# Optimization experiments

Measured on AMD Instinct MI355X. Metric: run time of the kernel, lower is better.

## Reference

```python
import jax, jax.numpy as jnp
import numpy as np
import math

D_MODEL = 768
NHEAD = 12
D_HEAD = D_MODEL // NHEAD
TAU = 300.0
NEG = -1e9

def setup_inputs() -> dict:
    key = jax.random.key(0)
    ks = jax.random.split(key, 12)
    N, L, D = 64, 512, D_MODEL
    tokens = jax.random.normal(ks[0], (N, L, D), dtype=jnp.float32)
    ts = jax.random.uniform(ks[1], (N, L, 1), dtype=jnp.float32) * 3600.0  # seconds in a 1h window
    mask = jnp.ones((N, L, 1), dtype=jnp.float32)
    s = 1.0 / math.sqrt(D)
    Wq = jax.random.normal(ks[2], (D, D), dtype=jnp.float32) * s
    bq = jnp.zeros((D,), dtype=jnp.float32)
    Wk = jax.random.normal(ks[3], (D, D), dtype=jnp.float32) * s
    bk = jnp.zeros((D,), dtype=jnp.float32)
    Wv = jax.random.normal(ks[4], (D, D), dtype=jnp.float32) * s
    bv = jnp.zeros((D,), dtype=jnp.float32)
    Wo = jax.random.normal(ks[5], (D, D), dtype=jnp.float32) * s
    bo = jnp.zeros((D,), dtype=jnp.float32)
    readout = jax.random.normal(ks[6], (1, 1, D), dtype=jnp.float32)
    return dict(tokens=tokens, ts=ts, mask=mask, Wq=Wq, bq=bq, Wk=Wk, bk=bk,
                Wv=Wv, bv=bv, Wo=Wo, bo=bo, readout=readout)

def _heads(x, N, L):
    return x.reshape(N, L, NHEAD, D_HEAD).transpose(0, 2, 1, 3)  # (N,H,L,dh)

def reference(tokens, ts, mask, Wq, bq, Wk, bk, Wv, bv, Wo, bo, readout):
    N, L, D = tokens.shape
    scale = 1.0 / math.sqrt(D_HEAD)
    # time-decay bias: log(exp(-|dt|/tau) + 1e-12)
    t = (ts - ts[:, :1, :])[..., 0]                       # (N,L)
    dt = jnp.abs(t[:, :, None] - t[:, None, :])           # (N,L,L)
    bias = jnp.log(jnp.exp(-dt / max(TAU, 1e-6)) + 1e-12)
    q = _heads(tokens @ Wq.T + bq, N, L)
    k = _heads(tokens @ Wk.T + bk, N, L)
    v = _heads(tokens @ Wv.T + bv, N, L)
    attn = jnp.einsum('nhqd,nhkd->nhqk', q, k) * scale + bias[:, None, :, :]
    key_pad = mask[..., 0] <= 0                           # (N,L)
    attn = jnp.where(key_pad[:, None, None, :], NEG, attn)
    A = jax.nn.softmax(attn, axis=-1)
    out = jnp.einsum('nhqk,nhkd->nhqd', A, v).transpose(0, 2, 1, 3).reshape(N, L, D)
    out = (out @ Wo.T + bo) * mask
    # readout pooling attention (single learned query)
    qh = jnp.broadcast_to(readout, (N, 1, D)).reshape(N, 1, NHEAD, D_HEAD).transpose(0, 2, 1, 3)
    kh = _heads(out, N, L)
    pool = jnp.einsum('nhqd,nhkd->nhqk', qh, kh) * scale  # (N,H,1,L)
    pool = jnp.where(key_pad[:, None, None, :], NEG, pool)
    P = jax.nn.softmax(pool, axis=-1)
    pooled = jnp.einsum('nhqk,nhkd->nhqd', P, kh).transpose(0, 2, 1, 3).reshape(N, 1, D)
    return pooled[:, 0, :]
```

## Files before the change

kernel.cpp:

```cpp
#include <hip/hip_runtime.h>
#include <stdint.h>

#define AS1 __attribute__((address_space(1)))
#define AS3 __attribute__((address_space(3)))

typedef __bf16 bf16x8 __attribute__((ext_vector_type(8)));
typedef float  f32x4  __attribute__((ext_vector_type(4)));
typedef float  f32x16 __attribute__((ext_vector_type(16)));

#define MFMA16(a, b, c) __builtin_amdgcn_mfma_f32_16x16x32_bf16((a), (b), (c), 0, 0, 0)
#define MFMA32(a, b, c) __builtin_amdgcn_mfma_f32_32x32x16_bf16((a), (b), (c), 0, 0, 0)

#define SEQ   512
#define NBAT  64
#define DM    768
#define NH    12
#define DH    64
#define NQKV  2304
#define NTOK  (NBAT * SEQ)
#define NKB   12

__device__ __forceinline__ uint16_t f2bf(float x) {
  uint32_t u = __float_as_uint(x);
  return (uint16_t)((u + 0x7FFFu + ((u >> 16) & 1u)) >> 16);
}

__device__ __forceinline__ void async16(uint16_t* lds, const uint16_t* g) {
  __builtin_amdgcn_global_load_lds((AS1 void*)(uintptr_t)(const void*)g,
                                   (AS3 void*)lds, 16, 0, 0);
}

__device__ __forceinline__ int swz(int r) { return (r ^ (r >> 3)) & 7; }

__global__ __launch_bounds__(256) void k_cvt(
    const float* __restrict__ tokens,
    const float* __restrict__ Wq, const float* __restrict__ Wk,
    const float* __restrict__ Wv, const float* __restrict__ Wo,
    const float* __restrict__ bq, const float* __restrict__ bk, const float* __restrict__ bv,
    uint16_t* __restrict__ X, uint16_t* __restrict__ Wqkv_pk, uint16_t* __restrict__ Wob_pk,
    float* __restrict__ bqkv) {
  int i = blockIdx.x * 256 + threadIdx.x;
  {
    const float4* sp = (const float4*)tokens;
    float4 a = sp[2 * i], b = sp[2 * i + 1];
    union { uint16_t u[8]; uint4 v; } o;
    o.u[0] = f2bf(a.x); o.u[1] = f2bf(a.y); o.u[2] = f2bf(a.z); o.u[3] = f2bf(a.w);
    o.u[4] = f2bf(b.x); o.u[5] = f2bf(b.y); o.u[6] = f2bf(b.z); o.u[7] = f2bf(b.w);
    ((uint4*)X)[i] = o.v;
  }
  if (i < 221184) {
    int lane = i & 63, ks = (i >> 6) & 3, kb = (i >> 8) % NKB, g = i / 3072;
    int row = g * 32 + (lane & 31);
    int k   = kb * 64 + ks * 16 + (lane >> 5) * 8;
    const float* src = (row < 768)  ? Wq + (size_t)row * 768 + k
                     : (row < 1536) ? Wk + (size_t)(row - 768) * 768 + k
                                    : Wv + (size_t)(row - 1536) * 768 + k;
    float4 a = *(const float4*)src, b = *(const float4*)(src + 4);
    union { uint16_t u[8]; uint4 v; } o;
    o.u[0] = f2bf(a.x); o.u[1] = f2bf(a.y); o.u[2] = f2bf(a.z); o.u[3] = f2bf(a.w);
    o.u[4] = f2bf(b.x); o.u[5] = f2bf(b.y); o.u[6] = f2bf(b.z); o.u[7] = f2bf(b.w);
    ((uint4*)Wqkv_pk)[i] = o.v;
  }
  if (i < 73728) {
    int lane = i & 63, ks = (i >> 6) & 3, kb = (i >> 8) % NKB, g = i / 3072;
    int row = g * 32 + (lane & 31);
    int k   = kb * 64 + ks * 16 + (lane >> 5) * 8;
    const float* src = Wo + (size_t)row * 768 + k;
    float4 a = *(const float4*)src, b = *(const float4*)(src + 4);
    union { uint16_t u[8]; uint4 v; } o;
    o.u[0] = f2bf(a.x); o.u[1] = f2bf(a.y); o.u[2] = f2bf(a.z); o.u[3] = f2bf(a.w);
    o.u[4] = f2bf(b.x); o.u[5] = f2bf(b.y); o.u[6] = f2bf(b.z); o.u[7] = f2bf(b.w);
    ((uint4*)Wob_pk)[i] = o.v;
  }
  if (i < 768) { bqkv[i] = bq[i]; bqkv[i + 768] = bk[i]; bqkv[i + 1536] = bv[i]; }
}

__global__ __launch_bounds__(256) void k_gemm_bt(
    const uint16_t* __restrict__ A, const uint16_t* __restrict__ Bpk,
    const float* __restrict__ bias, const float* __restrict__ rowscale,
    uint16_t* __restrict__ C, int ldc, int ncol) {
  __shared__ uint16_t Alds[128 * 64];
  const int tid  = threadIdx.x;
  const int w    = tid >> 6, lane = tid & 63;
  const int wu   = __builtin_amdgcn_readfirstlane(w);
  const int l32  = lane & 31, kh = lane >> 5;
  const int sup  = blockIdx.x / (32 * ncol);
  const int t    = blockIdx.x % (32 * ncol);
  const int row0 = (sup * 32 + (t & 31)) * 128, col0 = (t >> 5) * 128;
  const int wrow = (w >> 1) * 64,   wcol = (w & 1) * 64;

  const uint16_t* bw = Bpk + (size_t)((col0 >> 5) + (w & 1) * 2) * (NKB * 2048) + lane * 8;

  f32x16 acc[2][2] = {};
  for (int kb = 0; kb < NKB; ++kb) {
    bf16x8 bfr[4][2];
#pragma unroll
    for (int ks = 0; ks < 4; ++ks)
#pragma unroll
      for (int nt = 0; nt < 2; ++nt)
        bfr[ks][nt] = *(const bf16x8*)(bw + (size_t)nt * (NKB * 2048) + (kb * 4 + ks) * 512);
    __syncthreads();
#pragma unroll
    for (int j = 0; j < 4; ++j) {
      int cid = j * 256 + w * 64 + lane;
      int r = cid >> 3, cc = cid & 7, c = cc ^ swz(r);
      async16(&Alds[(j * 256 + wu * 64) * 8],
              A + (size_t)(row0 + r) * 768 + kb * 64 + c * 8);
    }
    __syncthreads();
#pragma unroll
    for (int ks = 0; ks < 4; ++ks) {
      bf16x8 af[2];
#pragma unroll
      for (int mt = 0; mt < 2; ++mt) {
        int r = wrow + mt * 32 + l32;
        int c = (ks * 2 + kh) ^ swz(r);
        af[mt] = *(const bf16x8*)&Alds[r * 64 + c * 8];
      }
#pragma unroll
      for (int mt = 0; mt < 2; ++mt)
#pragma unroll
        for (int nt = 0; nt < 2; ++nt)
          acc[mt][nt] = MFMA32(af[mt], bfr[ks][nt], acc[mt][nt]);
    }
  }
#pragma unroll
  for (int nt = 0; nt < 2; ++nt) {
    int col = col0 + wcol + nt * 32 + l32;
    float bv = bias[col];
#pragma unroll
    for (int mt = 0; mt < 2; ++mt) {
#pragma unroll
      for (int rg = 0; rg < 16; ++rg) {
        int row = row0 + wrow + mt * 32 + (rg & 3) + 8 * (rg >> 2) + 4 * kh;
        float v = acc[mt][nt][rg] + bv;
        if (rowscale) v *= rowscale[row];
        C[(size_t)row * ldc + col] = f2bf(v);
      }
    }
  }
}

__global__ __launch_bounds__(256) void k_attn(
    const uint16_t* __restrict__ QKV, const float* __restrict__ ts,
    const float* __restrict__ mask, uint16_t* __restrict__ Aout) {
  __shared__ uint16_t Klds[64 * 64];
  __shared__ uint16_t Vt[64 * 72];
  __shared__ uint16_t Plds[4][32 * 72];
  __shared__ float tkl[SEQ];

  const int tid = threadIdx.x, w = tid >> 6, lane = tid & 63;
  const int wu = __builtin_amdgcn_readfirstlane(w);
  const int quad = lane >> 4, l16 = lane & 15;
  int b = blockIdx.x;
  int xcd = b & 7, i = b >> 3;
  int qt = i & 3;
  int hg = xcd * 96 + (i >> 2);
  int n = hg / NH, h = hg % NH;
  const int q0 = qt * 128 + w * 32;
  const size_t rowbase = (size_t)n * SEQ * NQKV;

  const float c1 = 0.125f * 1.44269504f;
  const float c2 = 1.44269504f / 300.0f;

  for (int l = tid; l < SEQ; l += 256) {
    float t = ts[n * SEQ + l] * c2;
    tkl[l] = (mask[n * SEQ + l] > 0.f) ? t : 3e38f;
  }

  bf16x8 qf[2][2];
  float tq[2][4];
#pragma unroll
  for (int qs = 0; qs < 2; ++qs) {
    int qr = q0 + qs * 16 + l16;
    const uint16_t* qp = QKV + rowbase + (size_t)qr * NQKV + h * DH;
#pragma unroll
    for (int dsp = 0; dsp < 2; ++dsp)
      qf[qs][dsp] = *(const bf16x8*)(qp + dsp * 32 + quad * 8);
#pragma unroll
    for (int rg = 0; rg < 4; ++rg)
      tq[qs][rg] = ts[n * SEQ + q0 + qs * 16 + quad * 4 + rg] * c2;
  }

  f32x4 accO[2][4] = {};
  f32x4 accL[2] = {};
  bf16x8 ones_b;
  {
    union { uint16_t u[8]; bf16x8 v; } t;
    uint16_t o = (l16 == 0) ? 0x3F80 : 0;
#pragma unroll
    for (int j = 0; j < 8; ++j) t.u[j] = o;
    ones_b = t.v;
  }
  uint16_t* Pw = &Plds[w][0];

  for (int k0 = 0; k0 < SEQ; k0 += 64) {
    __syncthreads();
#pragma unroll
    for (int j = 0; j < 2; ++j) {
      int cid = j * 256 + w * 64 + lane;
      int r = cid >> 3, cc = cid & 7, c = cc ^ swz(r);
      const uint16_t* g = QKV + rowbase + (size_t)(k0 + r) * NQKV + DM + h * DH + c * 8;
      async16(&Klds[(j * 256 + wu * 64) * 8], g);
    }
    {
      int r = tid & 63, db = (tid >> 6) * 16;
      const uint16_t* g = QKV + rowbase + (size_t)(k0 + r) * NQKV + 2 * DM + h * DH + db;
      union { uint4 v; uint16_t u[8]; } a0, a1;
      a0.v = *(const uint4*)g;
      a1.v = *(const uint4*)(g + 8);
#pragma unroll
      for (int j = 0; j < 8; ++j) Vt[(db + j) * 72 + r] = a0.u[j];
#pragma unroll
      for (int j = 0; j < 8; ++j) Vt[(db + 8 + j) * 72 + r] = a1.u[j];
    }
    __syncthreads();

#pragma unroll
    for (int kt = 0; kt < 2; ++kt) {
      f32x4 s[2][2] = {};
#pragma unroll
      for (int dsp = 0; dsp < 2; ++dsp) {
        bf16x8 kf[2];
#pragma unroll
        for (int ksu = 0; ksu < 2; ++ksu) {
          int r = kt * 32 + 2 * l16 + ksu;
          int c = (dsp * 4 + quad) ^ swz(r);
          kf[ksu] = *(const bf16x8*)&Klds[r * 64 + c * 8];
        }
#pragma unroll
        for (int qs = 0; qs < 2; ++qs)
#pragma unroll
          for (int ksu = 0; ksu < 2; ++ksu)
            s[qs][ksu] = MFMA16(qf[qs][dsp], kf[ksu], s[qs][ksu]);
      }
      float tk0 = tkl[k0 + kt * 32 + 2 * l16];
      float tk1 = tkl[k0 + kt * 32 + 2 * l16 + 1];
#pragma unroll
      for (int qs = 0; qs < 2; ++qs) {
#pragma unroll
        for (int rg = 0; rg < 4; ++rg) {
          float d0 = fabsf(tq[qs][rg] - tk0);
          float d1 = fabsf(tq[qs][rg] - tk1);
          float p0 = __builtin_amdgcn_exp2f(fmaf(s[qs][0][rg], c1, -d0));
          float p1 = __builtin_amdgcn_exp2f(fmaf(s[qs][1][rg], c1, -d1));
          uint32_t u = (__float_as_uint(p0) >> 16) | (__float_as_uint(p1) & 0xFFFF0000u);
          *(uint32_t*)(Pw + (qs * 16 + quad * 4 + rg) * 72 + kt * 32 + 2 * l16) = u;
        }
      }
      bf16x8 vb[4];
#pragma unroll
      for (int dt = 0; dt < 4; ++dt)
        vb[dt] = *(const bf16x8*)&Vt[(dt * 16 + l16) * 72 + kt * 32 + quad * 8];
#pragma unroll
      for (int qs = 0; qs < 2; ++qs) {
        bf16x8 pa = *(const bf16x8*)(Pw + (qs * 16 + l16) * 72 + kt * 32 + quad * 8);
#pragma unroll
        for (int dt = 0; dt < 4; ++dt)
          accO[qs][dt] = MFMA16(pa, vb[dt], accO[qs][dt]);
        accL[qs] = MFMA16(pa, ones_b, accL[qs]);
      }
    }
  }
#pragma unroll
  for (int qs = 0; qs < 2; ++qs) {
    float inv[4];
#pragma unroll
    for (int rg = 0; rg < 4; ++rg) {
      float lv = __shfl(accL[qs][rg], lane & 48, 64);
      inv[rg] = 1.0f / lv;
    }
#pragma unroll
    for (int dt = 0; dt < 4; ++dt) {
#pragma unroll
      for (int rg = 0; rg < 4; ++rg) {
        int qr = q0 + qs * 16 + quad * 4 + rg;
        float v = accO[qs][dt][rg] * inv[rg];
        Aout[(size_t)(n * SEQ + qr) * DM + h * DH + dt * 16 + l16] = f2bf(v);
      }
    }
  }
}

__global__ __launch_bounds__(256) void k_pool(
    const uint16_t* __restrict__ Out, const float* __restrict__ mask,
    const float* __restrict__ readout, float* __restrict__ dst) {
  __shared__ float rsl[64];
  __shared__ float ex[SEQ];
  __shared__ float red[4];
  __shared__ float part[8][64];
  int b = blockIdx.x;
  int n = b / NH, h = b % NH;
  int tid = threadIdx.x;
  if (tid < 64) rsl[tid] = readout[h * DH + tid];
  __syncthreads();

  float suml = 0.f;
  for (int l = tid; l < SEQ; l += 256) {
    const uint16_t* rowp = Out + (size_t)(n * SEQ + l) * DM + h * DH;
    float acc = 0.f;
#pragma unroll
    for (int c = 0; c < 8; ++c) {
      union { uint4 v; uint16_t u[8]; } t;
      t.v = *(const uint4*)(rowp + c * 8);
#pragma unroll
      for (int j = 0; j < 8; ++j)
        acc += __uint_as_float(((uint32_t)t.u[j]) << 16) * rsl[c * 8 + j];
    }
    float e = __builtin_amdgcn_exp2f(acc * (0.125f * 1.44269504f));
    e = (mask[n * SEQ + l] > 0.f) ? e : 0.f;
    ex[l] = e;
    suml += e;
  }
#pragma unroll
  for (int off = 32; off; off >>= 1) suml += __shfl_down(suml, off, 64);
  if ((tid & 63) == 0) red[tid >> 6] = suml;
  __syncthreads();
  float inv = 1.0f / (red[0] + red[1] + red[2] + red[3]);

  int d0 = (tid & 31) * 2, ch = tid >> 5;
  float a0 = 0.f, a1 = 0.f;
  for (int l = ch * 64; l < ch * 64 + 64; ++l) {
    uint32_t pv = *(const uint32_t*)(Out + (size_t)(n * SEQ + l) * DM + h * DH + d0);
    float e = ex[l];
    a0 = fmaf(__uint_as_float(pv << 16), e, a0);
    a1 = fmaf(__uint_as_float(pv & 0xFFFF0000u), e, a1);
  }
  part[ch][d0] = a0;
  part[ch][d0 + 1] = a1;
  __syncthreads();
  if (tid < 64) {
    float s = 0.f;
#pragma unroll
    for (int c = 0; c < 8; ++c) s += part[c][tid];
    dst[n * DM + h * DH + tid] = s * inv;
  }
}

extern "C" void kernel_launch(void* const* d_in, const int* in_sizes, int n_in,
                              void* d_out, int out_size, void* d_ws, size_t ws_size,
                              hipStream_t stream) {
  const float* tokens  = (const float*)d_in[0];
  const float* ts      = (const float*)d_in[1];
  const float* mask    = (const float*)d_in[2];
  const float* Wq      = (const float*)d_in[3];
  const float* bq      = (const float*)d_in[4];
  const float* Wk      = (const float*)d_in[5];
  const float* bk      = (const float*)d_in[6];
  const float* Wv      = (const float*)d_in[7];
  const float* bv      = (const float*)d_in[8];
  const float* Wo      = (const float*)d_in[9];
  const float* bo      = (const float*)d_in[10];
  const float* readout = (const float*)d_in[11];

  char* ws = (char*)d_ws;
  uint16_t* X    = (uint16_t*)ws;
  uint16_t* Wqkv = (uint16_t*)(ws + 50331648);
  uint16_t* Wob  = (uint16_t*)(ws + 53870592);
  float*    bqkv = (float*)   (ws + 55050240);
  uint16_t* QKV  = (uint16_t*)(ws + 55059456);
  uint16_t* attn = X;
  uint16_t* Outb = QKV;

  k_cvt<<<12288, 256, 0, stream>>>(tokens, Wq, Wk, Wv, Wo, bq, bk, bv, X, Wqkv, Wob, bqkv);
  k_gemm_bt<<<4608, 256, 0, stream>>>(X, Wqkv, bqkv, nullptr, QKV, NQKV, 18);
  k_attn<<<3072, 256, 0, stream>>>(QKV, ts, mask, attn);
  k_gemm_bt<<<1536, 256, 0, stream>>>(attn, Wob, bo, mask, Outb, DM, 6);
  k_pool<<<768, 256, 0, stream>>>(Outb, mask, readout, (float*)d_out);
}
```

Before: 496.6 us.

## Pre-pack GEMM A operands into MFMA fragment layout and drop LDS staging

The token conversion kernel and the attention output now write activations in the same packed per-lane MFMA fragment layout already used for weights. The GEMM then loads both A and B fragments straight from global memory into registers, with no LDS staging and no barriers. This removes the shared-memory round trip and the syncthreads in the GEMM inner loop. The cost is that every A fragment is re-read from global or L2 by each wave that needs it, with no sharing through LDS. The attention kernel's output stores also become scattered 2-byte writes in the packed layout, and the tokens conversion now reads its input strided.

```diff
diff --git a/kernel.cpp b/kernel.cpp
--- a/kernel.cpp
+++ b/kernel.cpp
@@ -19,6 +19,7 @@
 #define NQKV  2304
 #define NTOK  (NBAT * SEQ)
 #define NKB   12
+#define GS    (NKB * 2048)
 
 __device__ __forceinline__ uint16_t f2bf(float x) {
   uint32_t u = __float_as_uint(x);
@@ -31,30 +32,31 @@
 }
 
 __device__ __forceinline__ int swz(int r) { return (r ^ (r >> 3)) & 7; }
+
 
 __global__ __launch_bounds__(256) void k_cvt(
     const float* __restrict__ tokens,
     const float* __restrict__ Wq, const float* __restrict__ Wk,
     const float* __restrict__ Wv, const float* __restrict__ Wo,
     const float* __restrict__ bq, const float* __restrict__ bk, const float* __restrict__ bv,
-    uint16_t* __restrict__ X, uint16_t* __restrict__ Wqkv_pk, uint16_t* __restrict__ Wob_pk,
+    uint16_t* __restrict__ Xpk, uint16_t* __restrict__ Wqkv_pk, uint16_t* __restrict__ Wob_pk,
     float* __restrict__ bqkv) {
   int i = blockIdx.x * 256 + threadIdx.x;
+  int lane = i & 63, ks = (i >> 6) & 3, kb = (i >> 8) % NKB, g = i / 3072;
+  int r32 = lane & 31, kk = kb * 64 + ks * 16 + (lane >> 5) * 8;
   {
-    const float4* sp = (const float4*)tokens;
-    float4 a = sp[2 * i], b = sp[2 * i + 1];
+    const float* src = tokens + (size_t)(g * 32 + r32) * 768 + kk;
+    float4 a = *(const float4*)src, b = *(const float4*)(src + 4);
     union { uint16_t u[8]; uint4 v; } o;
     o.u[0] = f2bf(a.x); o.u[1] = f2bf(a.y); o.u[2] = f2bf(a.z); o.u[3] = f2bf(a.w);
     o.u[4] = f2bf(b.x); o.u[5] = f2bf(b.y); o.u[6] = f2bf(b.z); o.u[7] = f2bf(b.w);
-    ((uint4*)X)[i] = o.v;
+    ((uint4*)Xpk)[i] = o.v;
   }
   if (i < 221184) {
-    int lane = i & 63, ks = (i >> 6) & 3, kb = (i >> 8) % NKB, g = i / 3072;
-    int row = g * 32 + (lane & 31);
-    int k   = kb * 64 + ks * 16 + (lane >> 5) * 8;
-    const float* src = (row < 768)  ? Wq + (size_t)row * 768 + k
-                     : (row < 1536) ? Wk + (size_t)(row - 768) * 768 + k
-                                    : Wv + (size_t)(row - 1536) * 768 + k;
+    int row = g * 32 + r32;
+    const float* src = (row < 768)  ? Wq + (size_t)row * 768 + kk
+                     : (row < 1536) ? Wk + (size_t)(row - 768) * 768 + kk
+                                    : Wv + (size_t)(row - 1536) * 768 + kk;
     float4 a = *(const float4*)src, b = *(const float4*)(src + 4);
     union { uint16_t u[8]; uint4 v; } o;
     o.u[0] = f2bf(a.x); o.u[1] = f2bf(a.y); o.u[2] = f2bf(a.z); o.u[3] = f2bf(a.w);
@@ -62,10 +64,7 @@
     ((uint4*)Wqkv_pk)[i] = o.v;
   }
   if (i < 73728) {
-    int lane = i & 63, ks = (i >> 6) & 3, kb = (i >> 8) % NKB, g = i / 3072;
-    int row = g * 32 + (lane & 31);
-    int k   = kb * 64 + ks * 16 + (lane >> 5) * 8;
-    const float* src = Wo + (size_t)row * 768 + k;
+    const float* src = Wo + (size_t)(g * 32 + r32) * 768 + kk;
     float4 a = *(const float4*)src, b = *(const float4*)(src + 4);
     union { uint16_t u[8]; uint4 v; } o;
     o.u[0] = f2bf(a.x); o.u[1] = f2bf(a.y); o.u[2] = f2bf(a.z); o.u[3] = f2bf(a.w);
@@ -76,53 +75,38 @@
 }
 
 __global__ __launch_bounds__(256) void k_gemm_bt(
-    const uint16_t* __restrict__ A, const uint16_t* __restrict__ Bpk,
+    const uint16_t* __restrict__ Apk, const uint16_t* __restrict__ Bpk,
     const float* __restrict__ bias, const float* __restrict__ rowscale,
     uint16_t* __restrict__ C, int ldc, int ncol) {
-  __shared__ uint16_t Alds[128 * 64];
   const int tid  = threadIdx.x;
   const int w    = tid >> 6, lane = tid & 63;
-  const int wu   = __builtin_amdgcn_readfirstlane(w);
   const int l32  = lane & 31, kh = lane >> 5;
   const int sup  = blockIdx.x / (32 * ncol);
   const int t    = blockIdx.x % (32 * ncol);
   const int row0 = (sup * 32 + (t & 31)) * 128, col0 = (t >> 5) * 128;
   const int wrow = (w >> 1) * 64,   wcol = (w & 1) * 64;
 
-  const uint16_t* bw = Bpk + (size_t)((col0 >> 5) + (w & 1) * 2) * (NKB * 2048) + lane * 8;
+  const uint16_t* aw = Apk + ((size_t)(row0 >> 5) + (w >> 1) * 2) * GS + lane * 8;
+  const uint16_t* bw = Bpk + ((size_t)(col0 >> 5) + (w & 1) * 2) * GS + lane * 8;
 
   f32x16 acc[2][2] = {};
   for (int kb = 0; kb < NKB; ++kb) {
-    bf16x8 bfr[4][2];
+    bf16x8 af[4][2], bfr[4][2];
+#pragma unroll
+    for (int ks = 0; ks < 4; ++ks) {
+      int off = (kb * 4 + ks) * 512;
+#pragma unroll
+      for (int mt = 0; mt < 2; ++mt) af[ks][mt]  = *(const bf16x8*)(aw + (size_t)mt * GS + off);
+#pragma unroll
+      for (int nt = 0; nt < 2; ++nt) bfr[ks][nt] = *(const bf16x8*)(bw + (size_t)nt * GS + off);
+    }
 #pragma unroll
     for (int ks = 0; ks < 4; ++ks)
 #pragma unroll
-      for (int nt = 0; nt < 2; ++nt)
-        bfr[ks][nt] = *(const bf16x8*)(bw + (size_t)nt * (NKB * 2048) + (kb * 4 + ks) * 512);
-    __syncthreads();
-#pragma unroll
-    for (int j = 0; j < 4; ++j) {
-      int cid = j * 256 + w * 64 + lane;
-      int r = cid >> 3, cc = cid & 7, c = cc ^ swz(r);
-      async16(&Alds[(j * 256 + wu * 64) * 8],
-              A + (size_t)(row0 + r) * 768 + kb * 64 + c * 8);
-    }
-    __syncthreads();
-#pragma unroll
-    for (int ks = 0; ks < 4; ++ks) {
-      bf16x8 af[2];
-#pragma unroll
-      for (int mt = 0; mt < 2; ++mt) {
-        int r = wrow + mt * 32 + l32;
-        int c = (ks * 2 + kh) ^ swz(r);
-        af[mt] = *(const bf16x8*)&Alds[r * 64 + c * 8];
-      }
-#pragma unroll
       for (int mt = 0; mt < 2; ++mt)
 #pragma unroll
         for (int nt = 0; nt < 2; ++nt)
-          acc[mt][nt] = MFMA32(af[mt], bfr[ks][nt], acc[mt][nt]);
-    }
+          acc[mt][nt] = MFMA32(af[ks][mt], bfr[ks][nt], acc[mt][nt]);
   }
 #pragma unroll
   for (int nt = 0; nt < 2; ++nt) {
@@ -143,7 +127,7 @@
 
 __global__ __launch_bounds__(256) void k_attn(
     const uint16_t* __restrict__ QKV, const float* __restrict__ ts,
-    const float* __restrict__ mask, uint16_t* __restrict__ Aout) {
+    const float* __restrict__ mask, uint16_t* __restrict__ Apk_out) {
   __shared__ uint16_t Klds[64 * 64];
   __shared__ uint16_t Vt[64 * 72];
   __shared__ uint16_t Plds[4][32 * 72];
@@ -275,8 +259,10 @@
 #pragma unroll
       for (int rg = 0; rg < 4; ++rg) {
         int qr = q0 + qs * 16 + quad * 4 + rg;
+        int grow = n * 16 + (qr >> 5);
         float v = accO[qs][dt][rg] * inv[rg];
-        Aout[(size_t)(n * SEQ + qr) * DM + h * DH + dt * 16 + l16] = f2bf(v);
+        Apk_out[((size_t)(grow * NKB + h) * 4 + dt) * 512 +
+                ((l16 >> 3) * 32 + (qr & 31)) * 8 + (l16 & 7)] = f2bf(v);
       }
     }
   }
```

Result: slower. 524.7 us (+5.7%).

## Fuse token fp32-to-bf16 conversion into QKV GEMM A-tile loading

Applied to the files above, without the earlier changes.

The separate pass that converted all tokens to bf16 in the workspace is removed. A new QKV GEMM kernel reads fp32 tokens directly, converts them in registers and writes bf16 into LDS, and k_cvt now only packs weights. This drops a full write and re-read of the 50MB bf16 token copy. In exchange, each of the 18 column tiles rereads the fp32 A rows at twice the bytes, and the async global-to-LDS loads become synchronous register loads.

```diff
diff --git a/kernel.cpp b/kernel.cpp
--- a/kernel.cpp
+++ b/kernel.cpp
@@ -19,6 +19,7 @@
 #define NQKV  2304
 #define NTOK  (NBAT * SEQ)
 #define NKB   12
+#define GS    (NKB * 2048)
 
 __device__ __forceinline__ uint16_t f2bf(float x) {
   uint32_t u = __float_as_uint(x);
@@ -32,29 +33,21 @@
 
 __device__ __forceinline__ int swz(int r) { return (r ^ (r >> 3)) & 7; }
 
+
 __global__ __launch_bounds__(256) void k_cvt(
-    const float* __restrict__ tokens,
     const float* __restrict__ Wq, const float* __restrict__ Wk,
     const float* __restrict__ Wv, const float* __restrict__ Wo,
     const float* __restrict__ bq, const float* __restrict__ bk, const float* __restrict__ bv,
-    uint16_t* __restrict__ X, uint16_t* __restrict__ Wqkv_pk, uint16_t* __restrict__ Wob_pk,
+    uint16_t* __restrict__ Wqkv_pk, uint16_t* __restrict__ Wob_pk,
     float* __restrict__ bqkv) {
   int i = blockIdx.x * 256 + threadIdx.x;
+  int lane = i & 63, ks = (i >> 6) & 3, kb = (i >> 8) % NKB, g = i / 3072;
+  int r32 = lane & 31, kk = kb * 64 + ks * 16 + (lane >> 5) * 8;
   {
-    const float4* sp = (const float4*)tokens;
-    float4 a = sp[2 * i], b = sp[2 * i + 1];
-    union { uint16_t u[8]; uint4 v; } o;
-    o.u[0] = f2bf(a.x); o.u[1] = f2bf(a.y); o.u[2] = f2bf(a.z); o.u[3] = f2bf(a.w);
-    o.u[4] = f2bf(b.x); o.u[5] = f2bf(b.y); o.u[6] = f2bf(b.z); o.u[7] = f2bf(b.w);
-    ((uint4*)X)[i] = o.v;
-  }
-  if (i < 221184) {
-    int lane = i & 63, ks = (i >> 6) & 3, kb = (i >> 8) % NKB, g = i / 3072;
-    int row = g * 32 + (lane & 31);
-    int k   = kb * 64 + ks * 16 + (lane >> 5) * 8;
-    const float* src = (row < 768)  ? Wq + (size_t)row * 768 + k
-                     : (row < 1536) ? Wk + (size_t)(row - 768) * 768 + k
-                                    : Wv + (size_t)(row - 1536) * 768 + k;
+    int row = g * 32 + r32;
+    const float* src = (row < 768)  ? Wq + (size_t)row * 768 + kk
+                     : (row < 1536) ? Wk + (size_t)(row - 768) * 768 + kk
+                                    : Wv + (size_t)(row - 1536) * 768 + kk;
     float4 a = *(const float4*)src, b = *(const float4*)(src + 4);
     union { uint16_t u[8]; uint4 v; } o;
     o.u[0] = f2bf(a.x); o.u[1] = f2bf(a.y); o.u[2] = f2bf(a.z); o.u[3] = f2bf(a.w);
@@ -62,10 +55,7 @@
     ((uint4*)Wqkv_pk)[i] = o.v;
   }
   if (i < 73728) {
-    int lane = i & 63, ks = (i >> 6) & 3, kb = (i >> 8) % NKB, g = i / 3072;
-    int row = g * 32 + (lane & 31);
-    int k   = kb * 64 + ks * 16 + (lane >> 5) * 8;
-    const float* src = Wo + (size_t)row * 768 + k;
+    const float* src = Wo + (size_t)(g * 32 + r32) * 768 + kk;
     float4 a = *(const float4*)src, b = *(const float4*)(src + 4);
     union { uint16_t u[8]; uint4 v; } o;
     o.u[0] = f2bf(a.x); o.u[1] = f2bf(a.y); o.u[2] = f2bf(a.z); o.u[3] = f2bf(a.w);
@@ -73,6 +63,85 @@
     ((uint4*)Wob_pk)[i] = o.v;
   }
   if (i < 768) { bqkv[i] = bq[i]; bqkv[i + 768] = bk[i]; bqkv[i + 1536] = bv[i]; }
+}
+
+__global__ __launch_bounds__(256) void k_gemm_qkv(
+    const float* __restrict__ Afp, const uint16_t* __restrict__ Bpk,
+    const float* __restrict__ bias, uint16_t* __restrict__ C, int ldc, int ncol) {
+  __shared__ uint16_t Alds[128 * 64];
+  const int tid  = threadIdx.x;
+  const int w    = tid >> 6, lane = tid & 63;
+  const int l32  = lane & 31, kh = lane >> 5;
+  const int sup  = blockIdx.x / (32 * ncol);
+  const int t    = blockIdx.x % (32 * ncol);
+  const int row0 = (sup * 32 + (t & 31)) * 128, col0 = (t >> 5) * 128;
+  const int wrow = (w >> 1) * 64,   wcol = (w & 1) * 64;
+
+  const uint16_t* bw = Bpk + (size_t)((col0 >> 5) + (w & 1) * 2) * GS + lane * 8;
+
+  int cr[4], cc4[4];
+#pragma unroll
+  for (int j = 0; j < 4; ++j) {
+    int cid = j * 256 + w * 64 + lane;
+    cr[j] = cid >> 3; cc4[j] = cid & 7;
+  }
+
+  f32x16 acc[2][2] = {};
+  for (int kb = 0; kb < NKB; ++kb) {
+    bf16x8 bfr[4][2];
+#pragma unroll
+    for (int ks = 0; ks < 4; ++ks)
+#pragma unroll
+      for (int nt = 0; nt < 2; ++nt)
+        bfr[ks][nt] = *(const bf16x8*)(bw + (size_t)nt * GS + (kb * 4 + ks) * 512);
+    float4 st[4][2];
+#pragma unroll
+    for (int j = 0; j < 4; ++j) {
+      int c = cc4[j] ^ swz(cr[j]);
+      const float* g = Afp + (size_t)(row0 + cr[j]) * 768 + kb * 64 + c * 8;
+      st[j][0] = *(const float4*)g;
+      st[j][1] = *(const float4*)(g + 4);
+    }
+    __syncthreads();
+#pragma unroll
+    for (int j = 0; j < 4; ++j) {
+      union { uint16_t u[8]; uint4 v; } o;
+      o.u[0] = f2bf(st[j][0].x); o.u[1] = f2bf(st[j][0].y);
+      o.u[2] = f2bf(st[j][0].z); o.u[3] = f2bf(st[j][0].w);
+      o.u[4] = f2bf(st[j][1].x); o.u[5] = f2bf(st[j][1].y);
+      o.u[6] = f2bf(st[j][1].z); o.u[7] = f2bf(st[j][1].w);
+      *(uint4*)&Alds[cr[j] * 64 + cc4[j] * 8] = o.v;
+    }
+    __syncthreads();
+#pragma unroll
+    for (int ks = 0; ks < 4; ++ks) {
+      bf16x8 af[2];
+#pragma unroll
+      for (int mt = 0; mt < 2; ++mt) {
+        int r = wrow + mt * 32 + l32;
+        int c = (ks * 2 + kh) ^ swz(r);
+        af[mt] = *(const bf16x8*)&Alds[r * 64 + c * 8];
+      }
+#pragma unroll
+      for (int mt = 0; mt < 2; ++mt)
+#pragma unroll
+        for (int nt = 0; nt < 2; ++nt)
+          acc[mt][nt] = MFMA32(af[mt], bfr[ks][nt], acc[mt][nt]);
+    }
+  }
+#pragma unroll
+  for (int nt = 0; nt < 2; ++nt) {
+    int col = col0 + wcol + nt * 32 + l32;
+    float bv = bias[col];
+#pragma unroll
+    for (int mt = 0; mt < 2; ++mt) {
+#pragma unroll
+      for (int rg = 0; rg < 16; ++rg) {
+        int row = row0 + wrow + mt * 32 + (rg & 3) + 8 * (rg >> 2) + 4 * kh;
+        C[(size_t)row * ldc + col] = f2bf(acc[mt][nt][rg] + bv);
+      }
+    }
+  }
 }
 
 __global__ __launch_bounds__(256) void k_gemm_bt(
@@ -89,7 +158,7 @@
   const int row0 = (sup * 32 + (t & 31)) * 128, col0 = (t >> 5) * 128;
   const int wrow = (w >> 1) * 64,   wcol = (w & 1) * 64;
 
-  const uint16_t* bw = Bpk + (size_t)((col0 >> 5) + (w & 1) * 2) * (NKB * 2048) + lane * 8;
+  const uint16_t* bw = Bpk + (size_t)((col0 >> 5) + (w & 1) * 2) * GS + lane * 8;
 
   f32x16 acc[2][2] = {};
   for (int kb = 0; kb < NKB; ++kb) {
@@ -98,7 +167,7 @@
     for (int ks = 0; ks < 4; ++ks)
 #pragma unroll
       for (int nt = 0; nt < 2; ++nt)
-        bfr[ks][nt] = *(const bf16x8*)(bw + (size_t)nt * (NKB * 2048) + (kb * 4 + ks) * 512);
+        bfr[ks][nt] = *(const bf16x8*)(bw + (size_t)nt * GS + (kb * 4 + ks) * 512);
     __syncthreads();
 #pragma unroll
     for (int j = 0; j < 4; ++j) {
@@ -354,17 +423,16 @@
   const float* readout = (const float*)d_in[11];
 
   char* ws = (char*)d_ws;
-  uint16_t* X    = (uint16_t*)ws;
+  uint16_t* Aout = (uint16_t*)ws;
   uint16_t* Wqkv = (uint16_t*)(ws + 50331648);
   uint16_t* Wob  = (uint16_t*)(ws + 53870592);
   float*    bqkv = (float*)   (ws + 55050240);
   uint16_t* QKV  = (uint16_t*)(ws + 55059456);
-  uint16_t* attn = X;
   uint16_t* Outb = QKV;
 
-  k_cvt<<<12288, 256, 0, stream>>>(tokens, Wq, Wk, Wv, Wo, bq, bk, bv, X, Wqkv, Wob, bqkv);
-  k_gemm_bt<<<4608, 256, 0, stream>>>(X, Wqkv, bqkv, nullptr, QKV, NQKV, 18);
-  k_attn<<<3072, 256, 0, stream>>>(QKV, ts, mask, attn);
-  k_gemm_bt<<<1536, 256, 0, stream>>>(attn, Wob, bo, mask, Outb, DM, 6);
+  k_cvt<<<864, 256, 0, stream>>>(Wq, Wk, Wv, Wo, bq, bk, bv, Wqkv, Wob, bqkv);
+  k_gemm_qkv<<<4608, 256, 0, stream>>>(tokens, Wqkv, bqkv, QKV, NQKV, 18);
+  k_attn<<<3072, 256, 0, stream>>>(QKV, ts, mask, Aout);
+  k_gemm_bt<<<1536, 256, 0, stream>>>(Aout, Wob, bo, mask, Outb, DM, 6);
   k_pool<<<768, 256, 0, stream>>>(Outb, mask, readout, (float*)d_out);
 }
```

After: 550.5 us. 1.11x slower.
